# Performance work log

Hardware: AMD Instinct MI355X
Metric: run time of the kernel (lower is better)

## Reference

```python
import jax, jax.numpy as jnp
import numpy as np

# Block-sparse causal local attention (DeepSpeed SparseSelfAttention math):
#   scores = SDD(Q, K^T) on nonzero layout blocks
#   scores = masked_fill(block-causal mask == 0, -inf)
#   probs  = sparse_softmax(scores * head_dim**-0.5)  (rpe=None, key_padding_mask=None)
#   out    = DSD(probs, V)
# Layout: block (i, j) is nonzero iff 0 <= i - j < W (causal sliding window of W blocks).

BSZ, H, S, D = 2, 8, 4096, 64
BLK = 32          # sparsity block size
W = 16            # number of local key blocks per query block (512-token window)


def setup_inputs() -> dict:
    key = jax.random.key(0)
    kq, kk, kv = jax.random.split(key, 3)
    query = jax.random.normal(kq, (BSZ, H, S, D), jnp.float32)
    k = jax.random.normal(kk, (BSZ, H, S, D), jnp.float32)
    v = jax.random.normal(kv, (BSZ, H, S, D), jnp.float32)
    return {"query": query, "key": k, "value": v}


def reference(query, key, value):
    b, h, s, d = query.shape
    nb = s // BLK
    scaling = float(d) ** -0.5

    qb = query.reshape(b, h, nb, BLK, d)
    kb = key.reshape(b, h, nb, BLK, d)
    vb = value.reshape(b, h, nb, BLK, d)

    blk_i = jnp.arange(nb)
    # key-block indices attended by each query block: i-W+1 ... i   [nb, W]
    k_idx = blk_i[:, None] + jnp.arange(-(W - 1), 1)[None, :]
    blk_valid = k_idx >= 0
    k_idx_c = jnp.maximum(k_idx, 0)

    Kg = kb[:, :, k_idx_c]   # [b, h, nb, W, BLK, d]
    Vg = vb[:, :, k_idx_c]   # [b, h, nb, W, BLK, d]

    # block-sparse SDD: only the W local blocks per query block are computed
    scores = jnp.einsum('bhnqd,bhnwkd->bhnqwk', qb, Kg) * scaling

    # token-level causal mask (covers the diagonal-block triangular mask
    # from make_sparse_attn_mask) + validity of gathered blocks
    qpos = blk_i[:, None] * BLK + jnp.arange(BLK)[None, :]           # [nb, BLK]
    kpos = k_idx_c[..., None] * BLK + jnp.arange(BLK)                # [nb, W, BLK]
    allowed = blk_valid[:, None, :, None] & (kpos[:, None, :, :] <= qpos[:, :, None, None])
    scores = jnp.where(allowed[None, None], scores, -jnp.inf)

    # fused sparse softmax over all present key positions of each query row
    probs = jax.nn.softmax(scores.reshape(b, h, nb, BLK, W * BLK), axis=-1)
    probs = probs.reshape(b, h, nb, BLK, W, BLK)

    # block-sparse DSD
    out = jnp.einsum('bhnqwk,bhnwkd->bhnqd', probs, Vg)
    return out.reshape(b, h, s, d)
```

## Files before the change

### kernel.cpp

```cpp
#include <hip/hip_runtime.h>
#include <hip/hip_bf16.h>


#define NH    8
#define SEQ   4096
#define DIM   64
#define NBLK  128
#define WIN   16
#define QG    2
#define GROUPS (NBLK / QG)

typedef __bf16 bf16x8 __attribute__((ext_vector_type(8)));
typedef __bf16 bf16x4 __attribute__((ext_vector_type(4)));
typedef float  f32x4  __attribute__((ext_vector_type(4)));
typedef unsigned short u16;
typedef unsigned int   u32;

#define KSTR 72
#define VSTR 40
#define DTHR 8.0f

__device__ __forceinline__ bf16x8 cvt8(f32x4 a, f32x4 b) {
    bf16x8 r;
#pragma unroll
    for (int j = 0; j < 4; ++j) { r[j] = (__bf16)a[j]; r[4 + j] = (__bf16)b[j]; }
    return r;
}

__global__ __launch_bounds__(256)
void sparse_attn_v18(const float* __restrict__ Q,
                     const float* __restrict__ K,
                     const float* __restrict__ V,
                     float* __restrict__ O)
{
    const int b  = (int)blockIdx.x;
    const int lg = (b & 7) * 128 + (b >> 3);
    const int bh = lg >> 6;
    const int n0 = (lg & 63) * QG;

    const int t    = (int)threadIdx.x;
    const int wave = t >> 6;
    const int lane = t & 63;
    const int l15  = lane & 15;
    const int l4   = lane >> 4;
    const int qi   = wave >> 1;
    const int rh   = wave & 1;
    const int nq   = n0 + qi;

    __shared__ u16 Kt[2][32][KSTR];
    __shared__ u16 Vt[2][64][VSTR];

    const size_t base = (size_t)bh * SEQ * DIM;
    const float SC = 0.125f * 1.44269504088896340736f;

    const int skrow = t >> 3;
    const int skc   = (t & 7) * 8;
    const int svkey = (t & 15) * 2;
    const int svdg  = t >> 4;

    bf16x8 qf[2];
    {
        const float* qp = Q + base + (size_t)(nq * 32 + rh * 16 + l15) * DIM + l4 * 8;
        f32x4 a0 = *(const f32x4*)qp        * SC;
        f32x4 b0 = *(const f32x4*)(qp + 4)  * SC;
        f32x4 a1 = *(const f32x4*)(qp + 32) * SC;
        f32x4 b1 = *(const f32x4*)(qp + 36) * SC;
        qf[0] = cvt8(a0, b0);
        qf[1] = cvt8(a1, b1);
    }

    f32x4 acc[4] = {};
    float m  = -1e30f;
    float lp = 0.f;

    const int lo  = (nq >= WIN - 1) ? nq - (WIN - 1) : 0;
    const int kb0 = (n0 >= WIN - 1) ? n0 - (WIN - 1) : 0;
    const int kb1 = n0 + QG - 1;

    f32x4 kra, krb, vra, vrb;
    {
        const float* kp = K + base + (size_t)(kb0 * 32 + skrow) * DIM + skc;
        kra = *(const f32x4*)kp;  krb = *(const f32x4*)(kp + 4);
        const float* vp = V + base + (size_t)(kb0 * 32 + svkey) * DIM + svdg * 4;
        vra = *(const f32x4*)vp;  vrb = *(const f32x4*)(vp + DIM);
    }
    {
        *(bf16x8*)&Kt[0][skrow][skc] = cvt8(kra, krb);
#pragma unroll
        for (int j = 0; j < 4; ++j) {
            u32 w = (u32)__builtin_bit_cast(u16, (__bf16)vra[j])
                  | ((u32)__builtin_bit_cast(u16, (__bf16)vrb[j]) << 16);
            *(u32*)&Vt[0][svdg * 4 + j][svkey] = w;
        }
    }
    __syncthreads();

    int cur = 0;
    for (int kb = kb0; kb <= kb1; ++kb) {
        const bool haveNext = (kb < kb1);

        if (haveNext) {
            const float* kp = K + base + (size_t)((kb + 1) * 32 + skrow) * DIM + skc;
            kra = *(const f32x4*)kp;  krb = *(const f32x4*)(kp + 4);
            const float* vp = V + base + (size_t)((kb + 1) * 32 + svkey) * DIM + svdg * 4;
            vra = *(const f32x4*)vp;  vrb = *(const f32x4*)(vp + DIM);
        }

        if (kb >= lo && kb <= nq) {
            bf16x8 kf[2][2];
#pragma unroll
            for (int kh = 0; kh < 2; ++kh)
#pragma unroll
                for (int c = 0; c < 2; ++c)
                    kf[kh][c] = *(const bf16x8*)&Kt[cur][kh * 16 + l15][c * 32 + l4 * 8];

            bf16x8 vf[4];
#pragma unroll
            for (int dt = 0; dt < 4; ++dt) {
                bf16x4 vlo = *(const bf16x4*)&Vt[cur][dt * 16 + l15][l4 * 4];
                bf16x4 vhi = *(const bf16x4*)&Vt[cur][dt * 16 + l15][16 + l4 * 4];
#pragma unroll
                for (int j = 0; j < 4; ++j) { vf[dt][j] = vlo[j]; vf[dt][4 + j] = vhi[j]; }
            }

            f32x4 s[2];
#pragma unroll
            for (int kh = 0; kh < 2; ++kh) {
                f32x4 a = {};
                a = __builtin_amdgcn_mfma_f32_16x16x32_bf16(kf[kh][0], qf[0], a, 0, 0, 0);
                a = __builtin_amdgcn_mfma_f32_16x16x32_bf16(kf[kh][1], qf[1], a, 0, 0, 0);
                s[kh] = a;
            }

            if (kb == nq) {
#pragma unroll
                for (int kh = 0; kh < 2; ++kh)
#pragma unroll
                    for (int r = 0; r < 4; ++r)
                        if (kh * 16 + l4 * 4 + r > rh * 16 + l15)
                            s[kh][r] = -1e30f;
            }

            bool ok = true;
#pragma unroll
            for (int kh = 0; kh < 2; ++kh)
#pragma unroll
                for (int r = 0; r < 4; ++r)
                    ok &= (s[kh][r] <= m + DTHR);

            if (!__all(ok)) {
                float t0 = -1e30f;
#pragma unroll
                for (int kh = 0; kh < 2; ++kh)
#pragma unroll
                    for (int r = 0; r < 4; ++r) t0 = fmaxf(t0, s[kh][r]);
                t0 = fmaxf(t0, __shfl_xor(t0, 16));
                t0 = fmaxf(t0, __shfl_xor(t0, 32));
                const float mn = fmaxf(m, t0);
                const float al = exp2f(m - mn);
                m = mn;
                lp *= al;
#pragma unroll
                for (int dt = 0; dt < 4; ++dt)
#pragma unroll
                    for (int r = 0; r < 4; ++r) acc[dt][r] *= al;
            }

            bf16x8 pbf;
            float psum = 0.f;
#pragma unroll
            for (int j = 0; j < 8; ++j) {
                const float pv = exp2f(s[j >> 2][j & 3] - m);
                psum += pv;
                pbf[j] = (__bf16)pv;
            }
            lp += psum;

#pragma unroll
            for (int dt = 0; dt < 4; ++dt)
                acc[dt] = __builtin_amdgcn_mfma_f32_16x16x32_bf16(
                    vf[dt], pbf, acc[dt], 0, 0, 0);
        }

        if (haveNext) {
            *(bf16x8*)&Kt[cur ^ 1][skrow][skc] = cvt8(kra, krb);
#pragma unroll
            for (int j = 0; j < 4; ++j) {
                u32 w = (u32)__builtin_bit_cast(u16, (__bf16)vra[j])
                      | ((u32)__builtin_bit_cast(u16, (__bf16)vrb[j]) << 16);
                *(u32*)&Vt[cur ^ 1][svdg * 4 + j][svkey] = w;
            }
        }

        __syncthreads();
        cur ^= 1;
    }

    {
        float ps = lp;
        ps += __shfl_xor(ps, 16);
        ps += __shfl_xor(ps, 32);
        const float inv = 1.0f / ps;
        float* op = O + base + (size_t)(nq * 32 + rh * 16 + l15) * DIM + l4 * 4;
#pragma unroll
        for (int dt = 0; dt < 4; ++dt) {
            f32x4 v;
#pragma unroll
            for (int r = 0; r < 4; ++r) v[r] = acc[dt][r] * inv;
            *(f32x4*)(op + dt * 16) = v;
        }
    }
}

extern "C" void kernel_launch(void* const* d_in, const int* in_sizes, int n_in,
                              void* d_out, int out_size, void* d_ws, size_t ws_size,
                              hipStream_t stream)
{
    const float* Q = (const float*)d_in[0];
    const float* K = (const float*)d_in[1];
    const float* V = (const float*)d_in[2];
    float*       O = (float*)d_out;

    const int nwg = 2 * NH * GROUPS;
    hipLaunchKernelGGL(sparse_attn_v18, dim3(nwg), dim3(256), 0, stream,
                       Q, K, V, O);
}
```

Before: 37.12 us.

## Group four query blocks per workgroup to share K/V tiles, permute V layout

Doubles the number of query blocks handled per workgroup (QG 2→4, 512 threads), so each staged K/V block in shared memory is reused by more query waves and total global K/V traffic drops. Staging loads are split across twice as many threads, and V is stored with a permuted key order so each lane reads its MFMA operand as a single 8-wide bf16 load instead of two 4-wide loads. The prefetch is made unconditional by clamping to the last block, which removes a branch but adds a redundant final load/store. The trade-off is half as many workgroups and a larger per-block thread count, which affects occupancy and load balance across CUs.

```diff
diff --git a/kernel.cpp b/kernel.cpp
--- a/kernel.cpp
+++ b/kernel.cpp
@@ -7,12 +7,13 @@
 #define DIM   64
 #define NBLK  128
 #define WIN   16
-#define QG    2
+#define QG    4
 #define GROUPS (NBLK / QG)
 
 typedef __bf16 bf16x8 __attribute__((ext_vector_type(8)));
 typedef __bf16 bf16x4 __attribute__((ext_vector_type(4)));
 typedef float  f32x4  __attribute__((ext_vector_type(4)));
+typedef float  f32x2  __attribute__((ext_vector_type(2)));
 typedef unsigned short u16;
 typedef unsigned int   u32;
 
@@ -20,23 +21,23 @@
 #define VSTR 40
 #define DTHR 8.0f
 
-__device__ __forceinline__ bf16x8 cvt8(f32x4 a, f32x4 b) {
-    bf16x8 r;
-#pragma unroll
-    for (int j = 0; j < 4; ++j) { r[j] = (__bf16)a[j]; r[4 + j] = (__bf16)b[j]; }
+__device__ __forceinline__ bf16x4 cvt4(f32x4 a) {
+    bf16x4 r;
+#pragma unroll
+    for (int j = 0; j < 4; ++j) r[j] = (__bf16)a[j];
     return r;
 }
 
-__global__ __launch_bounds__(256)
-void sparse_attn_v18(const float* __restrict__ Q,
+__global__ __launch_bounds__(512)
+void sparse_attn_v19(const float* __restrict__ Q,
                      const float* __restrict__ K,
                      const float* __restrict__ V,
                      float* __restrict__ O)
 {
     const int b  = (int)blockIdx.x;
-    const int lg = (b & 7) * 128 + (b >> 3);
-    const int bh = lg >> 6;
-    const int n0 = (lg & 63) * QG;
+    const int lg = (b & 7) * 64 + (b >> 3);
+    const int bh = lg >> 5;
+    const int n0 = (lg & 31) * QG;
 
     const int t    = (int)threadIdx.x;
     const int wave = t >> 6;
@@ -53,10 +54,11 @@
     const size_t base = (size_t)bh * SEQ * DIM;
     const float SC = 0.125f * 1.44269504088896340736f;
 
-    const int skrow = t >> 3;
-    const int skc   = (t & 7) * 8;
+    const int skrow = t >> 4;
+    const int skc   = (t & 15) * 4;
     const int svkey = (t & 15) * 2;
-    const int svdg  = t >> 4;
+    const int svd2  = t >> 4;
+    const int vp    = (svkey & 3) | (((svkey >> 2) & 3) << 3) | ((svkey >> 4) << 2);
 
     bf16x8 qf[2];
     {
@@ -65,8 +67,11 @@
         f32x4 b0 = *(const f32x4*)(qp + 4)  * SC;
         f32x4 a1 = *(const f32x4*)(qp + 32) * SC;
         f32x4 b1 = *(const f32x4*)(qp + 36) * SC;
-        qf[0] = cvt8(a0, b0);
-        qf[1] = cvt8(a1, b1);
+#pragma unroll
+        for (int j = 0; j < 4; ++j) {
+            qf[0][j] = (__bf16)a0[j]; qf[0][4 + j] = (__bf16)b0[j];
+            qf[1][j] = (__bf16)a1[j]; qf[1][4 + j] = (__bf16)b1[j];
+        }
     }
 
     f32x4 acc[4] = {};
@@ -77,33 +82,34 @@
     const int kb0 = (n0 >= WIN - 1) ? n0 - (WIN - 1) : 0;
     const int kb1 = n0 + QG - 1;
 
-    f32x4 kra, krb, vra, vrb;
+    f32x4 kr;  f32x2 va, vb;
     {
         const float* kp = K + base + (size_t)(kb0 * 32 + skrow) * DIM + skc;
-        kra = *(const f32x4*)kp;  krb = *(const f32x4*)(kp + 4);
-        const float* vp = V + base + (size_t)(kb0 * 32 + svkey) * DIM + svdg * 4;
-        vra = *(const f32x4*)vp;  vrb = *(const f32x4*)(vp + DIM);
-    }
-    {
-        *(bf16x8*)&Kt[0][skrow][skc] = cvt8(kra, krb);
-#pragma unroll
-        for (int j = 0; j < 4; ++j) {
-            u32 w = (u32)__builtin_bit_cast(u16, (__bf16)vra[j])
-                  | ((u32)__builtin_bit_cast(u16, (__bf16)vrb[j]) << 16);
-            *(u32*)&Vt[0][svdg * 4 + j][svkey] = w;
+        kr = *(const f32x4*)kp;
+        const float* vptr = V + base + (size_t)(kb0 * 32 + svkey) * DIM + svd2 * 2;
+        va = *(const f32x2*)vptr;
+        vb = *(const f32x2*)(vptr + DIM);
+    }
+    {
+        *(bf16x4*)&Kt[0][skrow][skc] = cvt4(kr);
+#pragma unroll
+        for (int j = 0; j < 2; ++j) {
+            u32 w = (u32)__builtin_bit_cast(u16, (__bf16)va[j])
+                  | ((u32)__builtin_bit_cast(u16, (__bf16)vb[j]) << 16);
+            *(u32*)&Vt[0][svd2 * 2 + j][vp] = w;
         }
     }
     __syncthreads();
 
     int cur = 0;
     for (int kb = kb0; kb <= kb1; ++kb) {
-        const bool haveNext = (kb < kb1);
-
-        if (haveNext) {
-            const float* kp = K + base + (size_t)((kb + 1) * 32 + skrow) * DIM + skc;
-            kra = *(const f32x4*)kp;  krb = *(const f32x4*)(kp + 4);
-            const float* vp = V + base + (size_t)((kb + 1) * 32 + svkey) * DIM + svdg * 4;
-            vra = *(const f32x4*)vp;  vrb = *(const f32x4*)(vp + DIM);
+        {
+            const int kn = (kb + 1 <= kb1) ? kb + 1 : kb1;
+            const float* kp = K + base + (size_t)(kn * 32 + skrow) * DIM + skc;
+            kr = *(const f32x4*)kp;
+            const float* vptr = V + base + (size_t)(kn * 32 + svkey) * DIM + svd2 * 2;
+            va = *(const f32x2*)vptr;
+            vb = *(const f32x2*)(vptr + DIM);
         }
 
         if (kb >= lo && kb <= nq) {
@@ -116,12 +122,8 @@
 
             bf16x8 vf[4];
 #pragma unroll
-            for (int dt = 0; dt < 4; ++dt) {
-                bf16x4 vlo = *(const bf16x4*)&Vt[cur][dt * 16 + l15][l4 * 4];
-                bf16x4 vhi = *(const bf16x4*)&Vt[cur][dt * 16 + l15][16 + l4 * 4];
-#pragma unroll
-                for (int j = 0; j < 4; ++j) { vf[dt][j] = vlo[j]; vf[dt][4 + j] = vhi[j]; }
-            }
+            for (int dt = 0; dt < 4; ++dt)
+                vf[dt] = *(const bf16x8*)&Vt[cur][dt * 16 + l15][l4 * 8];
 
             f32x4 s[2];
 #pragma unroll
@@ -182,13 +184,13 @@
                     vf[dt], pbf, acc[dt], 0, 0, 0);
         }
 
-        if (haveNext) {
-            *(bf16x8*)&Kt[cur ^ 1][skrow][skc] = cvt8(kra, krb);
-#pragma unroll
-            for (int j = 0; j < 4; ++j) {
-                u32 w = (u32)__builtin_bit_cast(u16, (__bf16)vra[j])
-                      | ((u32)__builtin_bit_cast(u16, (__bf16)vrb[j]) << 16);
-                *(u32*)&Vt[cur ^ 1][svdg * 4 + j][svkey] = w;
+        {
+            *(bf16x4*)&Kt[cur ^ 1][skrow][skc] = cvt4(kr);
+#pragma unroll
+            for (int j = 0; j < 2; ++j) {
+                u32 w = (u32)__builtin_bit_cast(u16, (__bf16)va[j])
+                      | ((u32)__builtin_bit_cast(u16, (__bf16)vb[j]) << 16);
+                *(u32*)&Vt[cur ^ 1][svd2 * 2 + j][vp] = w;
             }
         }
 
@@ -222,6 +224,6 @@
     float*       O = (float*)d_out;
 
     const int nwg = 2 * NH * GROUPS;
-    hipLaunchKernelGGL(sparse_attn_v18, dim3(nwg), dim3(256), 0, stream,
+    hipLaunchKernelGGL(sparse_attn_v19, dim3(nwg), dim3(512), 0, stream,
                        Q, K, V, O);
 }
```

New measurement: 33.95 us. 1.09x faster.
